# Kernel optimization log

Hardware: AMD Instinct MI355X
Metric: run time of the kernel (lower is better)

## Reference

```python
import jax, jax.numpy as jnp
import numpy as np

K = 3  # adaptive kernel size
M = 4  # channel reduction


def setup_inputs() -> dict:
    key = jax.random.key(0)
    ks = jax.random.split(key, 10)
    N, C, H, W = 32, 512, 48, 48
    Cm = C // M            # 128
    P = 512                # planes
    sc = 0.05
    x   = jax.random.normal(ks[0], (N, C, H, W), jnp.float32)
    Wc  = jax.random.normal(ks[1], (Cm, C), jnp.float32) * sc   # conv 1x1 (C->Cm)
    bc  = jax.random.normal(ks[2], (Cm,), jnp.float32) * sc
    Wkk = jax.random.normal(ks[3], (K * K,), jnp.float32) * sc  # conv_kernel (1->k*k, 1x1)
    bkk = jax.random.normal(ks[4], (K * K,), jnp.float32) * sc
    Wck = jax.random.normal(ks[5], (Cm, 2), jnp.float32) * sc   # conv_k (2->Cm, 1x1)
    bck = jax.random.normal(ks[6], (Cm,), jnp.float32) * sc
    b_ad = jax.random.normal(ks[7], (Cm,), jnp.float32) * sc    # conv_adap_kernel bias (learned)
    Wf  = jax.random.normal(ks[8], (P, Cm), jnp.float32) * sc   # fuse 1x1 (Cm->planes)
    bf  = jax.random.normal(ks[9], (P,), jnp.float32) * sc
    return {"x": x, "Wc": Wc, "bc": bc, "Wkk": Wkk, "bkk": bkk,
            "Wck": Wck, "bck": bck, "b_ad": b_ad, "Wf": Wf, "bf": bf}


def reference(x, Wc, bc, Wkk, bkk, Wck, bck, b_ad, Wf, bf):
    N, C, H, W = x.shape
    Cm = Wc.shape[0]
    k = K
    pad = (k - 1) // 2

    # f = relu(conv1x1(x)) -> [N, Cm, H, W]
    f = jax.nn.relu(jnp.einsum('oc,nchw->nohw', Wc, x) + bc[None, :, None, None])

    # global branch: adaptive avg pool to 1 -> shared conv1x1 -> relu -> [N, Cm]
    gk1 = jax.nn.relu(jnp.mean(x, axis=(2, 3)) @ Wc.T + bc)
    # conv_kernel (1->k*k 1x1 over permuted layout): per-channel affine into k*k values
    g_kern = (gk1[:, :, None] * Wkk[None, None, :] + bkk[None, None, :]).reshape(N, Cm, k, k)

    # spatial branch: adaptive max pool to k x k (H,W divisible by k) -> shared conv1x1 -> relu
    xm = x.reshape(N, C, k, H // k, k, W // k).max(axis=(3, 5))  # [N, C, k, k]
    sk = jax.nn.relu(jnp.einsum('oc,nckl->nokl', Wc, xm) + bc[None, :, None, None])

    # kernel generation: conv_k (2->Cm 1x1) over [g_kern, sk], then the permute makes
    # weight[o, c, :, :] = relu(sum_j Wck[o, j] * gs[c, j, :, :] + bck[o])
    gs = jnp.stack([g_kern, sk], axis=2)  # [N, Cm, 2, k, k]
    dynW = jax.nn.relu(jnp.einsum('oj,ncjkl->nockl', Wck, gs)
                       + bck[None, :, None, None, None])  # [N, Cm_out, Cm_in, k, k]

    # per-sample dynamic conv2d, vectorized over batch
    def conv_one(fn, wn):
        return jax.lax.conv_general_dilated(
            fn[None], wn, window_strides=(1, 1),
            padding=[(pad, pad), (pad, pad)])[0]

    y = jax.vmap(conv_one)(f, dynW) + b_ad[None, :, None, None]  # [N, Cm, H, W]

    # fuse 1x1 -> planes
    out = jnp.einsum('oc,nchw->nohw', Wf, y) + bf[None, :, None, None]
    return out
```

## Files before the change

### kernel.cpp

```cpp
#include <hip/hip_runtime.h>

#define N_   32
#define C_   512
#define CM_  128
#define H_   48
#define W_   48
#define HW_  (H_*W_)
#define P_   512

typedef unsigned short ushort_t;
typedef short s8v  __attribute__((ext_vector_type(8)));
typedef float f4v  __attribute__((ext_vector_type(4)));

__device__ __forceinline__ ushort_t f2bf(float x) {
    unsigned int u = __float_as_uint(x);
    u += 0x7fffu + ((u >> 16) & 1u);
    return (ushort_t)(u >> 16);
}

__global__ __launch_bounds__(256) void pool_kernel(const float* __restrict__ x,
                                                   float* __restrict__ meanx,
                                                   float* __restrict__ xm) {
    int plane = blockIdx.x;
    const float* base = x + (size_t)plane * HW_;
    int t = threadIdx.x;
    int r = t >> 4, cc = t & 15;
    float sum = 0.f;
    float mx[9];
#pragma unroll
    for (int b = 0; b < 9; ++b) {
        int h = (b / 3) * 16 + r;
        int w = (b % 3) * 16 + cc;
        float v = base[h * W_ + w];
        mx[b] = v;
        sum += v;
    }
#pragma unroll
    for (int off = 32; off > 0; off >>= 1) {
        sum += __shfl_down(sum, off);
#pragma unroll
        for (int b = 0; b < 9; ++b) mx[b] = fmaxf(mx[b], __shfl_down(mx[b], off));
    }
    __shared__ float s[4][10];
    int wave = t >> 6, lane = t & 63;
    if (lane == 0) {
#pragma unroll
        for (int b = 0; b < 9; ++b) s[wave][b] = mx[b];
        s[wave][9] = sum;
    }
    __syncthreads();
    if (t < 9) {
        float v = fmaxf(fmaxf(s[0][t], s[1][t]), fmaxf(s[2][t], s[3][t]));
        xm[(size_t)plane * 9 + t] = v;
    } else if (t == 9) {
        float v = s[0][9] + s[1][9] + s[2][9] + s[3][9];
        meanx[plane] = v * (1.0f / (float)HW_);
    }
}

__global__ __launch_bounds__(128) void branch_kernel(const float* __restrict__ meanx,
                                                     const float* __restrict__ xm,
                                                     const float* __restrict__ Wc,
                                                     const float* __restrict__ bc,
                                                     const float* __restrict__ Wkk,
                                                     const float* __restrict__ bkk,
                                                     float* __restrict__ gs) {
    int n = blockIdx.x;
    __shared__ float sin_[C_ * 10];
    int t = threadIdx.x;
    for (int i = t; i < C_ * 10; i += 128) {
        int c = i / 10, j = i % 10;
        sin_[i] = (j < 9) ? xm[((size_t)n * C_ + c) * 9 + j] : meanx[n * C_ + c];
    }
    __syncthreads();
    int o = t;
    float acc[10];
#pragma unroll
    for (int j = 0; j < 10; ++j) acc[j] = 0.f;
    const float* wrow = Wc + (size_t)o * C_;
    for (int c = 0; c < C_; ++c) {
        float wv = wrow[c];
        const float* in = &sin_[c * 10];
#pragma unroll
        for (int j = 0; j < 10; ++j) acc[j] += wv * in[j];
    }
    float bco = bc[o];
    float gk1 = fmaxf(acc[9] + bco, 0.f);
    size_t gbase = (size_t)n * 18 * CM_;
#pragma unroll
    for (int b = 0; b < 9; ++b) {
        gs[gbase + b * CM_ + o]       = gk1 * Wkk[b] + bkk[b];
        gs[gbase + (9 + b) * CM_ + o] = fmaxf(acc[b] + bco, 0.f);
    }
}

__global__ __launch_bounds__(256) void dynw_kernel(const float* __restrict__ gs,
                                                   const float* __restrict__ Wck,
                                                   const float* __restrict__ bck,
                                                   ushort_t* __restrict__ dynW_t) {
    int idx = blockIdx.x * 256 + threadIdx.x;
    int c8 = idx & 15;
    int o  = (idx >> 4) & 127;
    int v  = idx >> 11;
    int r  = v % 9;
    int n  = v / 9;
    const float* gp = gs + ((size_t)n * 18 + r) * CM_ + c8 * 8;
    float w0 = Wck[o * 2], w1 = Wck[o * 2 + 1], bk = bck[o];
    ushort_t u[8];
#pragma unroll
    for (int i = 0; i < 8; ++i) {
        float g = gp[i];
        float s = gp[9 * CM_ + i];
        u[i] = f2bf(fmaxf(w0 * g + w1 * s + bk, 0.f));
    }
    uint4 pk;
    pk.x = (unsigned)u[0] | ((unsigned)u[1] << 16);
    pk.y = (unsigned)u[2] | ((unsigned)u[3] << 16);
    pk.z = (unsigned)u[4] | ((unsigned)u[5] << 16);
    pk.w = (unsigned)u[6] | ((unsigned)u[7] << 16);
    *(uint4*)(dynW_t + (size_t)idx * 8) = pk;
}

__global__ __launch_bounds__(256) void convw_kernel(const float* __restrict__ Wc,
                                                    const float* __restrict__ Wf,
                                                    ushort_t* __restrict__ Wc_bf,
                                                    ushort_t* __restrict__ Wf_bf) {
    int idx = blockIdx.x * 256 + threadIdx.x;
    float4 v;
    ushort_t* dst;
    if (idx < 16384) {
        v = ((const float4*)Wc)[idx];
        dst = Wc_bf + (size_t)idx * 4;
    } else {
        int k = idx - 16384;
        v = ((const float4*)Wf)[k];
        dst = Wf_bf + (size_t)k * 4;
    }
    uint2 pk;
    pk.x = (unsigned)f2bf(v.x) | ((unsigned)f2bf(v.y) << 16);
    pk.y = (unsigned)f2bf(v.z) | ((unsigned)f2bf(v.w) << 16);
    *(uint2*)dst = pk;
}

__global__ __launch_bounds__(256) void fconv_mfma(const float* __restrict__ x,
                                                  const ushort_t* __restrict__ Wc_bf,
                                                  const float* __restrict__ bc,
                                                  ushort_t* __restrict__ f_t) {
    int n = blockIdx.y;
    int hw0 = blockIdx.x * 64;
    __shared__ ushort_t Bs[64 * 40];
    int t = threadIdx.x;
    int wave = t >> 6, lane = t & 63;
    int j = lane & 15, q = lane >> 4;
    int o_w = wave * 32;
    int sk  = t >> 4;
    int shw = (t & 15) * 4;

    const s8v* A = (const s8v*)Wc_bf;
    f4v acc[2][4];
#pragma unroll
    for (int mt = 0; mt < 2; ++mt)
#pragma unroll
        for (int nt = 0; nt < 4; ++nt) acc[mt][nt] = (f4v){0.f, 0.f, 0.f, 0.f};

    for (int c0 = 0; c0 < C_; c0 += 32) {
        const float* xr = x + ((size_t)n * C_ + c0 + 2 * sk) * HW_ + hw0 + shw;
        float4 v0 = *(const float4*)xr;
        float4 v1 = *(const float4*)(xr + HW_);
        __syncthreads();
        unsigned* Bw = (unsigned*)Bs;
        {
            unsigned w0 = (unsigned)f2bf(v0.x) | ((unsigned)f2bf(v1.x) << 16);
            unsigned w1 = (unsigned)f2bf(v0.y) | ((unsigned)f2bf(v1.y) << 16);
            unsigned w2 = (unsigned)f2bf(v0.z) | ((unsigned)f2bf(v1.z) << 16);
            unsigned w3 = (unsigned)f2bf(v0.w) | ((unsigned)f2bf(v1.w) << 16);
            Bw[(shw + 0) * 20 + sk] = w0;
            Bw[(shw + 1) * 20 + sk] = w1;
            Bw[(shw + 2) * 20 + sk] = w2;
            Bw[(shw + 3) * 20 + sk] = w3;
        }
        __syncthreads();
        s8v a0 = A[(size_t)(o_w + j) * 64 + (c0 >> 3) + q];
        s8v a1 = A[(size_t)(o_w + 16 + j) * 64 + (c0 >> 3) + q];
        s8v b[4];
#pragma unroll
        for (int nt = 0; nt < 4; ++nt)
            b[nt] = *(const s8v*)&Bs[(nt * 16 + j) * 40 + q * 8];
#pragma unroll
        for (int nt = 0; nt < 4; ++nt) {
            acc[0][nt] = __builtin_amdgcn_mfma_f32_16x16x32_bf16(a0, b[nt], acc[0][nt], 0, 0, 0);
            acc[1][nt] = __builtin_amdgcn_mfma_f32_16x16x32_bf16(a1, b[nt], acc[1][nt], 0, 0, 0);
        }
    }
#pragma unroll
    for (int mt = 0; mt < 2; ++mt) {
        int ob = o_w + mt * 16 + q * 4;
        float b4[4];
#pragma unroll
        for (int reg = 0; reg < 4; ++reg) b4[reg] = bc[ob + reg];
#pragma unroll
        for (int nt = 0; nt < 4; ++nt) {
            int hw = hw0 + nt * 16 + j;
            ushort_t u[4];
#pragma unroll
            for (int reg = 0; reg < 4; ++reg)
                u[reg] = f2bf(fmaxf(acc[mt][nt][reg] + b4[reg], 0.f));
            uint2 pk;
            pk.x = (unsigned)u[0] | ((unsigned)u[1] << 16);
            pk.y = (unsigned)u[2] | ((unsigned)u[3] << 16);
            *(uint2*)(f_t + ((size_t)n * HW_ + hw) * CM_ + ob) = pk;
        }
    }
}

__global__ __launch_bounds__(128) void dynconv_mfma(const ushort_t* __restrict__ f_t,
                                                    const ushort_t* __restrict__ dynW_t,
                                                    const float* __restrict__ b_ad,
                                                    ushort_t* __restrict__ y_bf) {
    int n  = blockIdx.z;
    int o0 = blockIdx.y * 64;
    int h0 = blockIdx.x * 4;
    int t = threadIdx.x;
    int wave = t >> 6, lane = t & 63;
    int j = lane & 15, q = lane >> 4;
    int rbase = h0 + wave * 2;

    const s8v* A = (const s8v*)dynW_t;
    const s8v* B = (const s8v*)f_t;
    size_t abase = (((size_t)n * 9) * 128 + o0 + j) * 16 + q;

    f4v acc[4][6];
#pragma unroll
    for (int mt = 0; mt < 4; ++mt)
#pragma unroll
        for (int nt = 0; nt < 6; ++nt) acc[mt][nt] = (f4v){0.f, 0.f, 0.f, 0.f};
    const s8v zero = (s8v)0;

    for (int cc = 0; cc < 4; ++cc) {
        for (int r = 0; r < 9; ++r) {
            int dh = r / 3 - 1, dw = r % 3 - 1;
            s8v a[4];
#pragma unroll
            for (int mt = 0; mt < 4; ++mt)
                a[mt] = A[abase + (size_t)r * 2048 + mt * 256 + cc * 4];
            s8v b[6];
#pragma unroll
            for (int rl = 0; rl < 2; ++rl) {
                int h = rbase + rl + dh;
                bool hok = (unsigned)h < (unsigned)H_;
#pragma unroll
                for (int wg = 0; wg < 3; ++wg) {
                    int w = wg * 16 + j + dw;
                    s8v v = zero;
                    if (hok && (unsigned)w < (unsigned)W_)
                        v = B[((size_t)n * HW_ + h * W_ + w) * 16 + q + cc * 4];
                    b[rl * 3 + wg] = v;
                }
            }
#pragma unroll
            for (int mt = 0; mt < 4; ++mt)
#pragma unroll
                for (int nt = 0; nt < 6; ++nt)
                    acc[mt][nt] = __builtin_amdgcn_mfma_f32_16x16x32_bf16(
                        a[mt], b[nt], acc[mt][nt], 0, 0, 0);
        }
    }
#pragma unroll
    for (int mt = 0; mt < 4; ++mt) {
        int ob = o0 + mt * 16 + q * 4;
        float ba[4];
#pragma unroll
        for (int reg = 0; reg < 4; ++reg) ba[reg] = b_ad[ob + reg];
#pragma unroll
        for (int rl = 0; rl < 2; ++rl) {
            int h = rbase + rl;
#pragma unroll
            for (int wg = 0; wg < 3; ++wg) {
                int nt = rl * 3 + wg;
                int hw = h * W_ + wg * 16 + j;
                ushort_t u[4];
#pragma unroll
                for (int reg = 0; reg < 4; ++reg)
                    u[reg] = f2bf(acc[mt][nt][reg] + ba[reg]);
                uint2 pk;
                pk.x = (unsigned)u[0] | ((unsigned)u[1] << 16);
                pk.y = (unsigned)u[2] | ((unsigned)u[3] << 16);
                *(uint2*)(y_bf + ((size_t)n * HW_ + hw) * CM_ + ob) = pk;
            }
        }
    }
}

__global__ __launch_bounds__(128) void fuse_mfma(const ushort_t* __restrict__ y_bf,
                                                 const ushort_t* __restrict__ Wf_bf,
                                                 const float* __restrict__ bf,
                                                 float* __restrict__ out) {
    int n  = blockIdx.z;
    int p0 = blockIdx.y * 64;
    int h0 = blockIdx.x * 4;
    int t = threadIdx.x;
    int wave = t >> 6, lane = t & 63;
    int j = lane & 15, q = lane >> 4;
    int rbase = h0 + wave * 2;

    const s8v* A = (const s8v*)Wf_bf;
    const s8v* B = (const s8v*)y_bf;

    f4v acc[4][6];
#pragma unroll
    for (int mt = 0; mt < 4; ++mt)
#pragma unroll
        for (int nt = 0; nt < 6; ++nt) acc[mt][nt] = (f4v){0.f, 0.f, 0.f, 0.f};

#pragma unroll
    for (int cc = 0; cc < 4; ++cc) {
        s8v a[4];
#pragma unroll
        for (int mt = 0; mt < 4; ++mt)
            a[mt] = A[(size_t)(p0 + mt * 16 + j) * 16 + cc * 4 + q];
        s8v b[6];
#pragma unroll
        for (int rl = 0; rl < 2; ++rl) {
            int h = rbase + rl;
#pragma unroll
            for (int wg = 0; wg < 3; ++wg) {
                int hw = h * W_ + wg * 16 + j;
                b[rl * 3 + wg] = B[((size_t)n * HW_ + hw) * 16 + cc * 4 + q];
            }
        }
#pragma unroll
        for (int mt = 0; mt < 4; ++mt)
#pragma unroll
            for (int nt = 0; nt < 6; ++nt)
                acc[mt][nt] = __builtin_amdgcn_mfma_f32_16x16x32_bf16(
                    a[mt], b[nt], acc[mt][nt], 0, 0, 0);
    }
#pragma unroll
    for (int mt = 0; mt < 4; ++mt) {
        int pb = p0 + mt * 16 + q * 4;
        float b4[4];
#pragma unroll
        for (int reg = 0; reg < 4; ++reg) b4[reg] = bf[pb + reg];
#pragma unroll
        for (int rl = 0; rl < 2; ++rl) {
            int h = rbase + rl;
#pragma unroll
            for (int wg = 0; wg < 3; ++wg) {
                int nt = rl * 3 + wg;
                int hw = h * W_ + wg * 16 + j;
#pragma unroll
                for (int reg = 0; reg < 4; ++reg)
                    out[((size_t)n * P_ + pb + reg) * HW_ + hw] = acc[mt][nt][reg] + b4[reg];
            }
        }
    }
}

extern "C" void kernel_launch(void* const* d_in, const int* in_sizes, int n_in,
                              void* d_out, int out_size, void* d_ws, size_t ws_size,
                              hipStream_t stream) {
    const float* x    = (const float*)d_in[0];
    const float* Wc   = (const float*)d_in[1];
    const float* bc   = (const float*)d_in[2];
    const float* Wkk  = (const float*)d_in[3];
    const float* bkk  = (const float*)d_in[4];
    const float* Wck  = (const float*)d_in[5];
    const float* bck  = (const float*)d_in[6];
    const float* b_ad = (const float*)d_in[7];
    const float* Wf   = (const float*)d_in[8];
    const float* bf   = (const float*)d_in[9];
    float* out = (float*)d_out;

    char* ws = (char*)d_ws;
    float*    meanx  = (float*)(ws);
    float*    xm     = (float*)(ws + 65536);
    float*    gs     = (float*)(ws + 655360);
    ushort_t* dynW_t = (ushort_t*)(ws + 950272);
    ushort_t* f_t    = (ushort_t*)(ws + 10387456);
    ushort_t* y_bf   = (ushort_t*)(ws + 29261824);
    ushort_t* Wc_bf  = (ushort_t*)(ws + 48136192);
    ushort_t* Wf_bf  = (ushort_t*)(ws + 48267264);

    hipLaunchKernelGGL(pool_kernel,    dim3(N_ * C_), dim3(256), 0, stream, x, meanx, xm);
    hipLaunchKernelGGL(branch_kernel,  dim3(N_),      dim3(128), 0, stream, meanx, xm, Wc, bc, Wkk, bkk, gs);
    hipLaunchKernelGGL(dynw_kernel,    dim3(2304),    dim3(256), 0, stream, gs, Wck, bck, dynW_t);
    hipLaunchKernelGGL(convw_kernel,   dim3(128),     dim3(256), 0, stream, Wc, Wf, Wc_bf, Wf_bf);
    hipLaunchKernelGGL(fconv_mfma,     dim3(36, 32),  dim3(256), 0, stream, x, Wc_bf, bc, f_t);
    hipLaunchKernelGGL(dynconv_mfma,   dim3(12, 2, 32), dim3(128), 0, stream, f_t, dynW_t, b_ad, y_bf);
    hipLaunchKernelGGL(fuse_mfma,      dim3(12, 8, 32), dim3(128), 0, stream, y_bf, Wf_bf, bf, out);
}
```

Measured before the change: 457.2 us.

## Stage dynamic-conv input rows in swizzled LDS with halo, reuse across taps

```diff
diff --git a/kernel.cpp b/kernel.cpp
--- a/kernel.cpp
+++ b/kernel.cpp
@@ -213,67 +213,93 @@
     }
 }
 
-__global__ __launch_bounds__(128) void dynconv_mfma(const ushort_t* __restrict__ f_t,
-                                                    const ushort_t* __restrict__ dynW_t,
-                                                    const float* __restrict__ b_ad,
-                                                    ushort_t* __restrict__ y_bf) {
-    int n  = blockIdx.z;
-    int o0 = blockIdx.y * 64;
-    int h0 = blockIdx.x * 4;
+__global__ __launch_bounds__(256, 3) void dynconv_mfma(const ushort_t* __restrict__ f_t,
+                                                       const ushort_t* __restrict__ dynW_t,
+                                                       const float* __restrict__ b_ad,
+                                                       ushort_t* __restrict__ y_bf) {
+    __shared__ ushort_t Bs[4 * 50 * 128];
+    int bid = blockIdx.x;
+    int vid = (bid & 7) * 96 + (bid >> 3);
+    int n   = vid / 24;
+    int h0  = (vid % 24) * 2;
     int t = threadIdx.x;
     int wave = t >> 6, lane = t & 63;
     int j = lane & 15, q = lane >> 4;
-    int rbase = h0 + wave * 2;
-
+
+    if (t < 128) {
+        int ri = t >> 5, wi = ((t >> 4) & 1) * 49, ci = t & 15;
+        int off = ((ri * 50 + wi) * 256 + ci * 16) ^ ((wi & 7) << 4);
+        uint4 z; z.x = 0u; z.y = 0u; z.z = 0u; z.w = 0u;
+        *(uint4*)((char*)Bs + off) = z;
+    }
+#pragma unroll
+    for (int ri = 0; ri < 4; ++ri) {
+        int h = h0 - 1 + ri;
+        bool hok = (unsigned)h < (unsigned)H_;
+        const uint4* src = (const uint4*)(f_t + ((size_t)n * HW_ + h * W_) * CM_);
+#pragma unroll
+        for (int s = 0; s < 3; ++s) {
+            int c2 = s * 256 + t;
+            int wi = (c2 >> 4) + 1, ci = c2 & 15;
+            uint4 v; v.x = 0u; v.y = 0u; v.z = 0u; v.w = 0u;
+            if (hok) v = src[c2];
+            int off = ((ri * 50 + wi) * 256 + ci * 16) ^ ((wi & 7) << 4);
+            *(uint4*)((char*)Bs + off) = v;
+        }
+    }
+    __syncthreads();
+
+    int ow = wave * 32;
     const s8v* A = (const s8v*)dynW_t;
-    const s8v* B = (const s8v*)f_t;
-    size_t abase = (((size_t)n * 9) * 128 + o0 + j) * 16 + q;
-
-    f4v acc[4][6];
-#pragma unroll
-    for (int mt = 0; mt < 4; ++mt)
+    size_t abase = ((size_t)n * 9 * 128 + ow + j) * 16 + q;
+
+    f4v acc[2][6];
+#pragma unroll
+    for (int mt = 0; mt < 2; ++mt)
 #pragma unroll
         for (int nt = 0; nt < 6; ++nt) acc[mt][nt] = (f4v){0.f, 0.f, 0.f, 0.f};
-    const s8v zero = (s8v)0;
 
     for (int cc = 0; cc < 4; ++cc) {
+        s8v a[9][2];
+#pragma unroll
         for (int r = 0; r < 9; ++r) {
-            int dh = r / 3 - 1, dw = r % 3 - 1;
-            s8v a[4];
-#pragma unroll
-            for (int mt = 0; mt < 4; ++mt)
-                a[mt] = A[abase + (size_t)r * 2048 + mt * 256 + cc * 4];
-            s8v b[6];
-#pragma unroll
-            for (int rl = 0; rl < 2; ++rl) {
-                int h = rbase + rl + dh;
-                bool hok = (unsigned)h < (unsigned)H_;
+            a[r][0] = A[abase + (size_t)r * 2048 + cc * 4];
+            a[r][1] = A[abase + (size_t)r * 2048 + 256 + cc * 4];
+        }
+#pragma unroll
+        for (int ri = 0; ri < 4; ++ri) {
+#pragma unroll
+            for (int dwi = 0; dwi < 3; ++dwi) {
+                int xr = ((j + dwi) & 7) << 4;
 #pragma unroll
                 for (int wg = 0; wg < 3; ++wg) {
-                    int w = wg * 16 + j + dw;
-                    s8v v = zero;
-                    if (hok && (unsigned)w < (unsigned)W_)
-                        v = B[((size_t)n * HW_ + h * W_ + w) * 16 + q + cc * 4];
-                    b[rl * 3 + wg] = v;
+                    int wi = wg * 16 + j + dwi;
+                    int off = ((ri * 50 + wi) * 256 + cc * 64 + q * 16) ^ xr;
+                    s8v b = *(const s8v*)((const char*)Bs + off);
+                    if (ri < 3) {
+                        int r = ri * 3 + dwi;
+                        acc[0][wg] = __builtin_amdgcn_mfma_f32_16x16x32_bf16(a[r][0], b, acc[0][wg], 0, 0, 0);
+                        acc[1][wg] = __builtin_amdgcn_mfma_f32_16x16x32_bf16(a[r][1], b, acc[1][wg], 0, 0, 0);
+                    }
+                    if (ri > 0) {
+                        int r = (ri - 1) * 3 + dwi;
+                        acc[0][3 + wg] = __builtin_amdgcn_mfma_f32_16x16x32_bf16(a[r][0], b, acc[0][3 + wg], 0, 0, 0);
+                        acc[1][3 + wg] = __builtin_amdgcn_mfma_f32_16x16x32_bf16(a[r][1], b, acc[1][3 + wg], 0, 0, 0);
+                    }
                 }
             }
-#pragma unroll
-            for (int mt = 0; mt < 4; ++mt)
-#pragma unroll
-                for (int nt = 0; nt < 6; ++nt)
-                    acc[mt][nt] = __builtin_amdgcn_mfma_f32_16x16x32_bf16(
-                        a[mt], b[nt], acc[mt][nt], 0, 0, 0);
-        }
-    }
-#pragma unroll
-    for (int mt = 0; mt < 4; ++mt) {
-        int ob = o0 + mt * 16 + q * 4;
+        }
+    }
+
+#pragma unroll
+    for (int mt = 0; mt < 2; ++mt) {
+        int ob = ow + mt * 16 + q * 4;
         float ba[4];
 #pragma unroll
         for (int reg = 0; reg < 4; ++reg) ba[reg] = b_ad[ob + reg];
 #pragma unroll
         for (int rl = 0; rl < 2; ++rl) {
-            int h = rbase + rl;
+            int h = h0 + rl;
 #pragma unroll
             for (int wg = 0; wg < 3; ++wg) {
                 int nt = rl * 3 + wg;
@@ -386,6 +412,6 @@
     hipLaunchKernelGGL(dynw_kernel,    dim3(2304),    dim3(256), 0, stream, gs, Wck, bck, dynW_t);
     hipLaunchKernelGGL(convw_kernel,   dim3(128),     dim3(256), 0, stream, Wc, Wf, Wc_bf, Wf_bf);
     hipLaunchKernelGGL(fconv_mfma,     dim3(36, 32),  dim3(256), 0, stream, x, Wc_bf, bc, f_t);
-    hipLaunchKernelGGL(dynconv_mfma,   dim3(12, 2, 32), dim3(128), 0, stream, f_t, dynW_t, b_ad, y_bf);
+    hipLaunchKernelGGL(dynconv_mfma,   dim3(768),     dim3(256), 0, stream, f_t, dynW_t, b_ad, y_bf);
     hipLaunchKernelGGL(fuse_mfma,      dim3(12, 8, 32), dim3(128), 0, stream, y_bf, Wf_bf, bf, out);
 }
```

Result: faster. 408.7 us (-10.6%).
